# Kernel tuning notes

Measured on AMD Instinct MI355X. Metric: run time of the kernel, lower is better.

Reference implementation:

```python
import jax, jax.numpy as jnp
import numpy as np

XYZ_MIN = jnp.array([-1.0, -1.0, -1.0], dtype=jnp.float32)
XYZ_MAX = jnp.array([1.0, 1.0, 1.0], dtype=jnp.float32)
ACT_SHIFT = float(np.log(1.0 / (1.0 - 1e-6) - 1.0))  # density bias shift
WS = 100  # world_size per axis for num_voxels=1024000 in [-1,1]^3
R, P = 4096, 128  # rays, points per ray


def grid_sample_3d(grid, xyz):
    """Trilinear grid_sample, align_corners=True, zeros padding.
    grid: [C, D, H, W] (D=z, H=y, W=x); xyz: [N, 3] world coords. Returns [N, C]."""
    C, D, H, W = grid.shape
    norm = (xyz - XYZ_MIN) / (XYZ_MAX - XYZ_MIN) * 2.0 - 1.0  # [-1,1]
    sizes = jnp.array([W, H, D], dtype=norm.dtype)
    pix = (norm + 1.0) * 0.5 * (sizes - 1.0)  # align_corners=True mapping
    p0f = jnp.floor(pix)
    frac = pix - p0f
    p0 = p0f.astype(jnp.int32)
    out = jnp.zeros((xyz.shape[0], C), dtype=grid.dtype)
    for dx in (0, 1):
        for dy in (0, 1):
            for dz in (0, 1):
                ix, iy, iz = p0[:, 0] + dx, p0[:, 1] + dy, p0[:, 2] + dz
                wx = frac[:, 0] if dx else 1.0 - frac[:, 0]
                wy = frac[:, 1] if dy else 1.0 - frac[:, 1]
                wz = frac[:, 2] if dz else 1.0 - frac[:, 2]
                valid = ((ix >= 0) & (ix < W) & (iy >= 0) & (iy < H)
                         & (iz >= 0) & (iz < D))
                ixc = jnp.clip(ix, 0, W - 1)
                iyc = jnp.clip(iy, 0, H - 1)
                izc = jnp.clip(iz, 0, D - 1)
                vals = grid[:, izc, iyc, ixc].T  # [N, C]
                out = out + vals * (wx * wy * wz * valid)[:, None]
    return out


def setup_inputs() -> dict:
    key = jax.random.key(0)
    ks = jax.random.split(key, 12)
    origins = jax.random.uniform(ks[0], (R, 3), jnp.float32, -0.5, 0.5)
    directions = jax.random.normal(ks[1], (R, 3), jnp.float32)
    lengths = jax.random.uniform(ks[2], (R, P), jnp.float32, 0.05, 0.6)
    grid_density = jax.random.normal(ks[3], (1, WS, WS, WS), jnp.float32) * 0.1
    grid_color = jax.random.normal(ks[4], (12, WS, WS, WS), jnp.float32) * 0.1
    d_in = 12 + 27
    w1 = jax.random.normal(ks[5], (d_in, 128), jnp.float32) / np.sqrt(d_in)
    b1 = jnp.zeros((128,), jnp.float32)
    w2 = jax.random.normal(ks[6], (128, 128), jnp.float32) / np.sqrt(128)
    b2 = jnp.zeros((128,), jnp.float32)
    w3 = jax.random.normal(ks[7], (128, 3), jnp.float32) / np.sqrt(128)
    b3 = jnp.zeros((3,), jnp.float32)
    return dict(origins=origins, directions=directions, lengths=lengths,
                grid_density=grid_density, grid_color=grid_color,
                w1=w1, b1=b1, w2=w2, b2=b2, w3=w3, b3=b3)


def reference(origins, directions, lengths, grid_density, grid_color,
              w1, b1, w2, b2, w3, b3):
    # ray points: [R, P, 3]
    pts = origins[:, None, :] + directions[:, None, :] * lengths[:, :, None]
    flat = pts.reshape(-1, 3)
    # density branch
    density = grid_sample_3d(grid_density, flat).reshape(R, P, 1)
    interval = jnp.linalg.norm(directions, axis=-1)[:, None, None]
    alpha = 1.0 - (1.0 + jnp.exp(density + ACT_SHIFT)) ** (-interval)
    # color branch: 12-ch feature grid + view-dir PE + small MLP
    color = grid_sample_3d(grid_color, flat).reshape(R, P, 12)
    freqs = jnp.array([1.0, 2.0, 4.0, 8.0], dtype=jnp.float32)
    emb = (directions[:, :, None] * freqs).reshape(R, 12)
    emb = jnp.concatenate([directions, jnp.sin(emb), jnp.cos(emb)], -1)  # [R,27]
    emb = jnp.broadcast_to(emb[:, None, :], (R, P, 27))
    h = jnp.concatenate([color, emb], -1)  # [R,P,39]
    h = jax.nn.relu(h @ w1 + b1)
    h = jax.nn.relu(h @ w2 + b2)
    rgb = jax.nn.sigmoid(h @ w3 + b3)
    return alpha, rgb
```

## Files before the change

kernel.cpp:

```cpp
#include <hip/hip_runtime.h>
#include <hip/hip_bf16.h>
#include <math.h>


typedef __bf16 bf16x4 __attribute__((ext_vector_type(4)));
typedef __bf16 bf16x8 __attribute__((ext_vector_type(8)));
typedef float  f32x4  __attribute__((ext_vector_type(4)));

#define ACT_SHIFT_F (-13.815509557964774f)

#define EMB_B   53248
#define PACK_B  315392
#define FEAT_B  32315392
#define NEED_FULL 49092608ull
#define NEED_PACK 32315392ull

__global__ __launch_bounds__(256)
void dvgo_prep(const float* __restrict__ g_gd, const float* __restrict__ g_gc,
               const float* __restrict__ g_w1, const float* __restrict__ g_w2,
               const float* __restrict__ g_w3, const float* __restrict__ g_dir,
               bf16x8* __restrict__ pack, __bf16* __restrict__ wsb,
               __bf16* __restrict__ emb, int wbase)
{
    const int bid = blockIdx.x;
    if (bid < wbase) {
        const int gi = bid * 256 + threadIdx.x;
        if (gi >= 1000000) return;
        bf16x8 v0, v1;
        #pragma unroll
        for (int c = 0; c < 8; ++c) v0[c] = (__bf16)g_gc[c * 1000000 + gi];
        #pragma unroll
        for (int c = 0; c < 4; ++c) v1[c] = (__bf16)g_gc[(8 + c) * 1000000 + gi];
        v1[4] = (__bf16)g_gd[gi];
        v1[5] = (__bf16)0.0f; v1[6] = (__bf16)0.0f; v1[7] = (__bf16)0.0f;
        pack[gi * 2 + 0] = v0;
        pack[gi * 2 + 1] = v1;
        return;
    }
    const int idx = (bid - wbase) * 256 + threadIdx.x;
    if (idx < 8192) {
        const int j = idx & 7, lane = (idx >> 3) & 63, ks = (idx >> 9) & 1, ct = idx >> 10;
        const int n = ct * 16 + (lane & 15);
        const int k = ks * 32 + ((lane >> 4) & 3) * 8 + j;
        wsb[idx] = (__bf16)((k < 39) ? g_w1[k * 128 + n] : 0.0f);
    } else if (idx < 24576) {
        const int i2 = idx - 8192;
        const int j = i2 & 7, lane = (i2 >> 3) & 63, ks = (i2 >> 9) & 3, ct = i2 >> 11;
        const int n = ct * 16 + (lane & 15);
        const int k = ks * 32 + ((lane >> 4) & 3) * 8 + j;
        wsb[idx] = (__bf16)g_w2[k * 128 + n];
    } else if (idx < 26624) {
        const int i3 = idx - 24576;
        const int j = i3 & 7, lane = (i3 >> 3) & 63, ks = i3 >> 9;
        const int c = lane & 15;
        const int k = ks * 32 + ((lane >> 4) & 3) * 8 + j;
        wsb[idx] = (__bf16)((c < 3) ? g_w3[k * 3 + c] : 0.0f);
    } else if (idx < 30720) {
        const int ray = idx - 26624;
        const float d0 = g_dir[ray*3+0], d1 = g_dir[ray*3+1], d2 = g_dir[ray*3+2];
        __bf16 e[32];
        #pragma unroll
        for (int s = 0; s < 32; ++s) e[s] = (__bf16)0.0f;
        #pragma unroll
        for (int m = 0; m < 12; ++m) {
            const int i = m >> 2, j = m & 3;
            const float di = (i == 0) ? d0 : ((i == 1) ? d1 : d2);
            const float a = di * (float)(1 << j);
            if (m >= 1) e[m - 1] = (__bf16)sinf(a);
            e[11 + m] = (__bf16)cosf(a);
        }
        bf16x8* o = (bf16x8*)(emb + (size_t)ray * 32);
        #pragma unroll
        for (int q = 0; q < 4; ++q) {
            bf16x8 v;
            #pragma unroll
            for (int j = 0; j < 8; ++j) v[j] = e[q*8 + j];
            o[q] = v;
        }
    }
}

__global__ __launch_bounds__(256, 6)
void dvgo_gather(const float* __restrict__ g_org, const float* __restrict__ g_dir,
                 const float* __restrict__ g_len, const bf16x8* __restrict__ pack,
                 __bf16* __restrict__ feat, float* __restrict__ out_alpha)
{
    const int pt  = blockIdx.x * 256 + threadIdx.x;
    const int ray = pt >> 7;
    const float d0 = g_dir[ray*3+0], d1 = g_dir[ray*3+1], d2 = g_dir[ray*3+2];
    const float o0 = g_org[ray*3+0], o1 = g_org[ray*3+1], o2 = g_org[ray*3+2];
    const float len = g_len[pt];

    const float px = (o0 + d0*len + 1.0f) * 49.5f;
    const float py = (o1 + d1*len + 1.0f) * 49.5f;
    const float pz = (o2 + d2*len + 1.0f) * 49.5f;
    const float fx = floorf(px), fy = floorf(py), fz = floorf(pz);
    const int ix = (int)fx, iy = (int)fy, iz = (int)fz;
    const float qx = px - fx, qy = py - fy, qz = pz - fz;
    const float wxa[2] = {1.0f - qx, qx};
    const float wya[2] = {1.0f - qy, qy};
    const float wza[2] = {1.0f - qz, qz};
    const int  cxa[2] = {min(max(ix,0),99),   min(max(ix+1,0),99)};
    const int  cya[2] = {min(max(iy,0),99),   min(max(iy+1,0),99)};
    const int  cza[2] = {min(max(iz,0),99),   min(max(iz+1,0),99)};
    const bool vxa[2] = {(unsigned)ix < 100u, (unsigned)(ix+1) < 100u};
    const bool vya[2] = {(unsigned)iy < 100u, (unsigned)(iy+1) < 100u};
    const bool vza[2] = {(unsigned)iz < 100u, (unsigned)(iz+1) < 100u};

    float den = 0.0f;
    float cc[12];
    #pragma unroll
    for (int c = 0; c < 12; ++c) cc[c] = 0.0f;

    #pragma unroll
    for (int dz = 0; dz < 2; ++dz)
    #pragma unroll
    for (int dy = 0; dy < 2; ++dy)
    #pragma unroll
    for (int dx = 0; dx < 2; ++dx) {
        float w = wxa[dx] * wya[dy] * wza[dz];
        if (!(vxa[dx] && vya[dy] && vza[dz])) w = 0.0f;
        const int gi = (cza[dz]*100 + cya[dy])*100 + cxa[dx];
        const bf16x8 v0 = pack[gi*2 + 0];
        const bf16x8 v1 = pack[gi*2 + 1];
        #pragma unroll
        for (int c = 0; c < 8; ++c) cc[c]     += w * (float)v0[c];
        #pragma unroll
        for (int c = 0; c < 4; ++c) cc[8 + c] += w * (float)v1[c];
        den += w * (float)v1[4];
    }

    const float interval = sqrtf(d0*d0 + d1*d1 + d2*d2);
    const float e = expf(den + ACT_SHIFT_F);
    out_alpha[pt] = -expm1f(-interval * log1pf(e));

    bf16x8 f0, f1;
    #pragma unroll
    for (int c = 0; c < 8; ++c) f0[c] = (__bf16)cc[c];
    #pragma unroll
    for (int c = 0; c < 4; ++c) f1[c] = (__bf16)cc[8 + c];
    f1[4] = (__bf16)d0; f1[5] = (__bf16)d1; f1[6] = (__bf16)d2;
    f1[7] = (__bf16)sinf(d0);
    bf16x8* fo = (bf16x8*)(feat + (size_t)pt * 16);
    fo[0] = f0;
    fo[1] = f1;
}

__global__ __launch_bounds__(256, 3)
void dvgo_mlp(const bf16x8* __restrict__ wf, const __bf16* __restrict__ emb,
              const __bf16* __restrict__ feat,
              const float* __restrict__ g_b1, const float* __restrict__ g_b2,
              const float* __restrict__ g_b3, float* __restrict__ out_rgb)
{
    __shared__ __align__(16) char smem[32768];
    const int tid  = threadIdx.x;
    const int ray  = blockIdx.x;
    const int lane = tid & 63;
    const int wid  = tid >> 6;
    const int lr   = lane & 15;
    const int lk   = lane >> 4;
    const int sz   = (lr & 7) << 4;

    int wb1[2];
    #pragma unroll
    for (int c2 = 0; c2 < 2; ++c2)
        wb1[c2] = lr*256 + ((((wid*2 + c2)*32) + lk*8) ^ sz);
    int rb2[4];
    #pragma unroll
    for (int ks = 0; ks < 4; ++ks)
        rb2[ks] = (wid*32 + lr)*256 + ((ks*64 + lk*16) ^ sz);
    const int rowb = (wid*32 + lr)*256;

    const bf16x8 ev = *(const bf16x8*)(emb + (size_t)ray*32 + (((lk + 2) & 3) * 8));
    bf16x8 zed;
    #pragma unroll
    for (int j = 0; j < 8; ++j) zed[j] = (__bf16)0.0f;
    const bf16x8 bq1 = (lk < 2) ? ev : zed;

    bf16x8 aw1[2][2];
    #pragma unroll
    for (int c2 = 0; c2 < 2; ++c2)
        #pragma unroll
        for (int ks = 0; ks < 2; ++ks)
            aw1[c2][ks] = wf[((wid*2 + c2)*2 + ks)*64 + lane];

    #pragma unroll
    for (int h = 0; h < 2; ++h) {
        bf16x8 ft[4];
        #pragma unroll
        for (int r4 = 0; r4 < 4; ++r4) {
            const int pt = ray*128 + (h*4 + r4)*16 + lr;
            ft[r4] = *(const bf16x8*)(feat + (size_t)pt*16 + (lk & 1)*8);
        }
        f32x4 acc1[4][2];
        #pragma unroll
        for (int r4 = 0; r4 < 4; ++r4)
            #pragma unroll
            for (int c2 = 0; c2 < 2; ++c2) acc1[r4][c2] = (f32x4){0.f,0.f,0.f,0.f};
        #pragma unroll
        for (int r4 = 0; r4 < 4; ++r4) {
            const bf16x8 b0 = (lk < 2) ? ft[r4] : ev;
            #pragma unroll
            for (int c2 = 0; c2 < 2; ++c2) {
                acc1[r4][c2] = __builtin_amdgcn_mfma_f32_16x16x32_bf16(aw1[c2][0], b0,  acc1[r4][c2], 0, 0, 0);
                acc1[r4][c2] = __builtin_amdgcn_mfma_f32_16x16x32_bf16(aw1[c2][1], bq1, acc1[r4][c2], 0, 0, 0);
            }
        }
        #pragma unroll
        for (int c2 = 0; c2 < 2; ++c2) {
            const f32x4 b1v = *(const f32x4*)(g_b1 + (wid*2 + c2)*16 + lk*4);
            #pragma unroll
            for (int r4 = 0; r4 < 4; ++r4) {
                bf16x4 hv;
                #pragma unroll
                for (int r = 0; r < 4; ++r)
                    hv[r] = (__bf16)fmaxf(acc1[r4][c2][r] + b1v[r], 0.0f);
                *(bf16x4*)(smem + wb1[c2] + (h*4 + r4)*4096) = hv;
            }
        }
    }
    __syncthreads();

    bf16x8 hq[2][4];
    #pragma unroll
    for (int q = 0; q < 2; ++q)
        #pragma unroll
        for (int ks = 0; ks < 4; ++ks)
            hq[q][ks] = *(const bf16x8*)(smem + rb2[ks] + q*4096);

    #pragma unroll
    for (int ct = 0; ct < 8; ++ct) {
        bf16x8 aw2[4];
        #pragma unroll
        for (int ks = 0; ks < 4; ++ks)
            aw2[ks] = wf[1024 + (ct*4 + ks)*64 + lane];
        f32x4 a0 = (f32x4){0.f,0.f,0.f,0.f};
        f32x4 a1 = (f32x4){0.f,0.f,0.f,0.f};
        #pragma unroll
        for (int ks = 0; ks < 4; ++ks) {
            a0 = __builtin_amdgcn_mfma_f32_16x16x32_bf16(aw2[ks], hq[0][ks], a0, 0, 0, 0);
            a1 = __builtin_amdgcn_mfma_f32_16x16x32_bf16(aw2[ks], hq[1][ks], a1, 0, 0, 0);
        }
        const f32x4 b2v = *(const f32x4*)(g_b2 + ct*16 + lk*4);
        bf16x4 h0, h1;
        #pragma unroll
        for (int r = 0; r < 4; ++r) {
            h0[r] = (__bf16)fmaxf(a0[r] + b2v[r], 0.0f);
            h1[r] = (__bf16)fmaxf(a1[r] + b2v[r], 0.0f);
        }
        const int csw = (ct*32 + lk*8) ^ sz;
        *(bf16x4*)(smem + rowb + csw) = h0;
        *(bf16x4*)(smem + rowb + 4096 + csw) = h1;
    }

    bf16x8 aw3[4];
    #pragma unroll
    for (int ks = 0; ks < 4; ++ks) aw3[ks] = wf[3072 + ks*64 + lane];
    f32x4 acc3[2];
    acc3[0] = (f32x4){0.f,0.f,0.f,0.f};
    acc3[1] = (f32x4){0.f,0.f,0.f,0.f};
    #pragma unroll
    for (int q = 0; q < 2; ++q)
        #pragma unroll
        for (int ks = 0; ks < 4; ++ks) {
            const bf16x8 hq3 = *(const bf16x8*)(smem + rb2[ks] + q*4096);
            acc3[q] = __builtin_amdgcn_mfma_f32_16x16x32_bf16(aw3[ks], hq3, acc3[q], 0, 0, 0);
        }

    float* smf = (float*)(smem + wid*8192);
    if (lk == 0) {
        const float b30 = g_b3[0], b31 = g_b3[1], b32 = g_b3[2];
        #pragma unroll
        for (int q = 0; q < 2; ++q) {
            const int o = (q*16 + lr)*3;
            smf[o + 0] = 1.0f / (1.0f + __expf(-(acc3[q][0] + b30)));
            smf[o + 1] = 1.0f / (1.0f + __expf(-(acc3[q][1] + b31)));
            smf[o + 2] = 1.0f / (1.0f + __expf(-(acc3[q][2] + b32)));
        }
    }
    asm volatile("s_waitcnt lgkmcnt(0)");
    __builtin_amdgcn_sched_barrier(0);
    {
        const int base = (ray*128 + wid*32)*3;
        out_rgb[base + lane] = smf[lane];
        if (lane < 32) out_rgb[base + 64 + lane] = smf[64 + lane];
    }
}

#define FB_FEAT_OFF 0
#define FB_PCC_OFF  16384
#define FB_H1_OFF   0
#define FB_PRGB_OFF 0

template <bool PACKED>
__global__ __launch_bounds__(256, 4)
void dvgo_main(const float* __restrict__ g_org, const float* __restrict__ g_dir,
               const float* __restrict__ g_len, const float* __restrict__ g_gd,
               const float* __restrict__ g_gc, const float* __restrict__ g_b1,
               const float* __restrict__ g_b2, const float* __restrict__ g_w3,
               const float* __restrict__ g_b3, const bf16x8* __restrict__ wf,
               const bf16x8* __restrict__ g_pack,
               float* __restrict__ out_alpha, float* __restrict__ out_rgb)
{
    __shared__ __align__(16) char smem[32768];
    float* smf = (float*)smem;
    const int tid = threadIdx.x;
    const int ray = blockIdx.x;
    const float d0 = g_dir[ray*3+0], d1 = g_dir[ray*3+1], d2 = g_dir[ray*3+2];
    {
        const float o0 = g_org[ray*3+0], o1 = g_org[ray*3+1], o2 = g_org[ray*3+2];
        const int p = tid & 127;
        const int dzv = tid >> 7;
        const float len = g_len[ray*128 + p];
        const float px = (o0 + d0*len + 1.0f) * 49.5f;
        const float py = (o1 + d1*len + 1.0f) * 49.5f;
        const float pz = (o2 + d2*len + 1.0f) * 49.5f;
        const float fx = floorf(px), fy = floorf(py), fz = floorf(pz);
        const int ix = (int)fx, iy = (int)fy, iz0 = (int)fz;
        const float qx = px - fx, qy = py - fy, qz = pz - fz;
        const float wxa[2] = {1.0f - qx, qx};
        const float wya[2] = {1.0f - qy, qy};
        const int  cxa[2] = {min(max(ix,0),99),   min(max(ix+1,0),99)};
        const int  cya[2] = {min(max(iy,0),99),   min(max(iy+1,0),99)};
        const bool vxa[2] = {(unsigned)ix < 100u, (unsigned)(ix+1) < 100u};
        const bool vya[2] = {(unsigned)iy < 100u, (unsigned)(iy+1) < 100u};
        const int  iz = iz0 + dzv;
        const float wz = dzv ? qz : (1.0f - qz);
        const int  cz = min(max(iz,0),99);
        const bool vz = (unsigned)iz < 100u;
        float den = 0.0f;
        float cc[12];
        #pragma unroll
        for (int c = 0; c < 12; ++c) cc[c] = 0.0f;
        #pragma unroll
        for (int dy = 0; dy < 2; ++dy)
        #pragma unroll
        for (int dx = 0; dx < 2; ++dx) {
            float w = wxa[dx] * wya[dy] * wz;
            if (!(vxa[dx] && vya[dy] && vz)) w = 0.0f;
            const int gi = (cz*100 + cya[dy])*100 + cxa[dx];
            if (PACKED) {
                const bf16x8 v0 = g_pack[gi*2 + 0];
                const bf16x8 v1 = g_pack[gi*2 + 1];
                #pragma unroll
                for (int c = 0; c < 8; ++c) cc[c]     += w * (float)v0[c];
                #pragma unroll
                for (int c = 0; c < 4; ++c) cc[8 + c] += w * (float)v1[c];
                den += w * (float)v1[4];
            } else {
                den += w * g_gd[gi];
                #pragma unroll
                for (int c = 0; c < 12; ++c) cc[c] += w * g_gc[c*1000000 + gi];
            }
        }
        if (dzv) {
            #pragma unroll
            for (int c = 0; c < 12; ++c) smf[FB_PCC_OFF/4 + p*13 + c] = cc[c];
            smf[FB_PCC_OFF/4 + p*13 + 12] = den;
        }
        __syncthreads();
        if (!dzv) {
            #pragma unroll
            for (int c = 0; c < 12; ++c) cc[c] += smf[FB_PCC_OFF/4 + p*13 + c];
            den += smf[FB_PCC_OFF/4 + p*13 + 12];
            const float interval = sqrtf(d0*d0 + d1*d1 + d2*d2);
            const float e = expf(den + ACT_SHIFT_F);
            out_alpha[ray*128 + p] = -expm1f(-interval * log1pf(e));
            bf16x8 f0; bf16x4 f1;
            #pragma unroll
            for (int c = 0; c < 8; ++c) f0[c] = (__bf16)cc[c];
            #pragma unroll
            for (int c = 0; c < 4; ++c) f1[c] = (__bf16)cc[8+c];
            const int swz = (p & 7) << 4;
            *reinterpret_cast<bf16x8*>(smem + ((FB_FEAT_OFF + p*128 +  0) ^ swz)) = f0;
            *reinterpret_cast<bf16x4*>(smem + ((FB_FEAT_OFF + p*128 + 16) ^ swz)) = f1;
        } else {
            float vals[52];
            vals[0] = d0; vals[1] = d1; vals[2] = d2;
            #pragma unroll
            for (int i = 0; i < 3; ++i) {
                const float di = (i == 0) ? d0 : ((i == 1) ? d1 : d2);
                #pragma unroll
                for (int j = 0; j < 4; ++j) {
                    const float a = di * (float)(1 << j);
                    vals[3  + i*4 + j] = sinf(a);
                    vals[15 + i*4 + j] = cosf(a);
                }
            }
            #pragma unroll
            for (int c = 27; c < 52; ++c) vals[c] = 0.0f;
            const int swz = (p & 7) << 4;
            #pragma unroll
            for (int i = 0; i < 13; ++i) {
                bf16x4 v4;
                #pragma unroll
                for (int r = 0; r < 4; ++r) v4[r] = (__bf16)vals[i*4 + r];
                *reinterpret_cast<bf16x4*>(smem + ((FB_FEAT_OFF + p*128 + 24 + i*8) ^ swz)) = v4;
            }
        }
    }
    __syncthreads();
    const int lane = tid & 63;
    const int wid  = tid >> 6;
    const int lr   = lane & 15;
    const int lk   = lane >> 4;
    {
        bf16x8 bf[2][2];
        #pragma unroll
        for (int rt = 0; rt < 2; ++rt)
            #pragma unroll
            for (int ks = 0; ks < 2; ++ks) {
                const int pt = wid*32 + rt*16 + lr;
                int a = FB_FEAT_OFF + pt*128 + ks*64 + lk*16; a ^= (pt & 7) << 4;
                bf[rt][ks] = *reinterpret_cast<const bf16x8*>(smem + a);
            }
        __syncthreads();
        f32x4 acc1[2][8];
        #pragma unroll
        for (int rt = 0; rt < 2; ++rt)
            #pragma unroll
            for (int ct = 0; ct < 8; ++ct) acc1[rt][ct] = (f32x4){0.f,0.f,0.f,0.f};
        #pragma unroll
        for (int ct = 0; ct < 8; ++ct) {
            const bf16x8 aw0 = wf[(ct*2 + 0)*64 + lane];
            const bf16x8 aw1 = wf[(ct*2 + 1)*64 + lane];
            #pragma unroll
            for (int rt = 0; rt < 2; ++rt) {
                acc1[rt][ct] = __builtin_amdgcn_mfma_f32_16x16x32_bf16(aw0, bf[rt][0], acc1[rt][ct], 0, 0, 0);
                acc1[rt][ct] = __builtin_amdgcn_mfma_f32_16x16x32_bf16(aw1, bf[rt][1], acc1[rt][ct], 0, 0, 0);
            }
        }
        #pragma unroll
        for (int ct = 0; ct < 8; ++ct) {
            const f32x4 b1v = *reinterpret_cast<const f32x4*>(g_b1 + ct*16 + lk*4);
            #pragma unroll
            for (int rt = 0; rt < 2; ++rt) {
                const int pt = wid*32 + rt*16 + lr;
                bf16x4 hv;
                #pragma unroll
                for (int r = 0; r < 4; ++r)
                    hv[r] = (__bf16)fmaxf(acc1[rt][ct][r] + b1v[r], 0.0f);
                int a = FB_H1_OFF + pt*256 + ct*32 + lk*8; a ^= (pt & 7) << 4;
                *reinterpret_cast<bf16x4*>(smem + a) = hv;
            }
        }
    }
    __syncthreads();
    const int wr = wid >> 1, wc = wid & 1;
    f32x4 acc2[4][4];
    #pragma unroll
    for (int rt = 0; rt < 4; ++rt)
        #pragma unroll
        for (int ct = 0; ct < 4; ++ct) acc2[rt][ct] = (f32x4){0.f,0.f,0.f,0.f};
    #pragma unroll
    for (int ks = 0; ks < 4; ++ks) {
        bf16x8 a2[4];
        #pragma unroll
        for (int rt = 0; rt < 4; ++rt) {
            const int pt = wr*64 + rt*16 + lr;
            int a = FB_H1_OFF + pt*256 + ks*64 + lk*16; a ^= (pt & 7) << 4;
            a2[rt] = *reinterpret_cast<const bf16x8*>(smem + a);
        }
        #pragma unroll
        for (int ct = 0; ct < 4; ++ct) {
            const int ctg = wc*4 + ct;
            const bf16x8 b2f = wf[1024 + (ctg*4 + ks)*64 + lane];
            #pragma unroll
            for (int rt = 0; rt < 4; ++rt)
                acc2[rt][ct] = __builtin_amdgcn_mfma_f32_16x16x32_bf16(a2[rt], b2f, acc2[rt][ct], 0, 0, 0);
        }
    }
    __syncthreads();
    {
        float b2v[4], w30[4], w31[4], w32[4];
        #pragma unroll
        for (int ct = 0; ct < 4; ++ct) {
            const int n2 = wc*64 + ct*16 + lr;
            b2v[ct] = g_b2[n2];
            w30[ct] = g_w3[n2*3 + 0];
            w31[ct] = g_w3[n2*3 + 1];
            w32[ct] = g_w3[n2*3 + 2];
        }
        #pragma unroll
        for (int rt = 0; rt < 4; ++rt)
            #pragma unroll
            for (int r = 0; r < 4; ++r) {
                float s0 = 0.f, s1 = 0.f, s2 = 0.f;
                #pragma unroll
                for (int ct = 0; ct < 4; ++ct) {
                    const float v = fmaxf(acc2[rt][ct][r] + b2v[ct], 0.0f);
                    s0 = fmaf(v, w30[ct], s0);
                    s1 = fmaf(v, w31[ct], s1);
                    s2 = fmaf(v, w32[ct], s2);
                }
                #pragma unroll
                for (int off = 1; off < 16; off <<= 1) {
                    s0 += __shfl_xor(s0, off);
                    s1 += __shfl_xor(s1, off);
                    s2 += __shfl_xor(s2, off);
                }
                if (lr == 0) {
                    const int pt = wr*64 + rt*16 + lk*4 + r;
                    const int base = FB_PRGB_OFF/4 + (wc*128 + pt)*3;
                    smf[base + 0] = s0;
                    smf[base + 1] = s1;
                    smf[base + 2] = s2;
                }
            }
    }
    __syncthreads();
    if (tid < 128) {
        const int p = tid;
        const float s0 = smf[p*3 + 0] + smf[(128 + p)*3 + 0] + g_b3[0];
        const float s1 = smf[p*3 + 1] + smf[(128 + p)*3 + 1] + g_b3[1];
        const float s2 = smf[p*3 + 2] + smf[(128 + p)*3 + 2] + g_b3[2];
        const int pt = ray*128 + p;
        out_rgb[pt*3 + 0] = 1.0f / (1.0f + expf(-s0));
        out_rgb[pt*3 + 1] = 1.0f / (1.0f + expf(-s1));
        out_rgb[pt*3 + 2] = 1.0f / (1.0f + expf(-s2));
    }
}

extern "C" void kernel_launch(void* const* d_in, const int* in_sizes, int n_in,
                              void* d_out, int out_size, void* d_ws, size_t ws_size,
                              hipStream_t stream)
{
    const float* g_org = (const float*)d_in[0];
    const float* g_dir = (const float*)d_in[1];
    const float* g_len = (const float*)d_in[2];
    const float* g_gd  = (const float*)d_in[3];
    const float* g_gc  = (const float*)d_in[4];
    const float* g_w1  = (const float*)d_in[5];
    const float* g_b1  = (const float*)d_in[6];
    const float* g_w2  = (const float*)d_in[7];
    const float* g_b2  = (const float*)d_in[8];
    const float* g_w3  = (const float*)d_in[9];
    const float* g_b3  = (const float*)d_in[10];
    float* out = (float*)d_out;

    __bf16* wsb  = (__bf16*)d_ws;
    __bf16* emb  = (__bf16*)((char*)d_ws + EMB_B);
    bf16x8* pack = (bf16x8*)((char*)d_ws + PACK_B);

    if (ws_size >= NEED_FULL) {
        __bf16* feat = (__bf16*)((char*)d_ws + FEAT_B);
        dvgo_prep<<<4027, 256, 0, stream>>>(g_gd, g_gc, g_w1, g_w2, g_w3, g_dir,
                                            pack, wsb, emb, 3907);
        dvgo_gather<<<2048, 256, 0, stream>>>(g_org, g_dir, g_len, pack, feat, out);
        dvgo_mlp<<<4096, 256, 0, stream>>>((const bf16x8*)wsb, emb, feat,
                                           g_b1, g_b2, g_b3, out + 4096*128);
    } else if (ws_size >= NEED_PACK) {
        dvgo_prep<<<4011, 256, 0, stream>>>(g_gd, g_gc, g_w1, g_w2, g_w3, g_dir,
                                            pack, wsb, emb, 3907);
        dvgo_main<true><<<4096, 256, 0, stream>>>(g_org, g_dir, g_len, g_gd, g_gc,
                                                  g_b1, g_b2, g_w3, g_b3,
                                                  (const bf16x8*)wsb, pack,
                                                  out, out + 4096*128);
    } else {
        dvgo_prep<<<104, 256, 0, stream>>>(g_gd, g_gc, g_w1, g_w2, g_w3, g_dir,
                                           pack, wsb, emb, 0);
        dvgo_main<false><<<4096, 256, 0, stream>>>(g_org, g_dir, g_len, g_gd, g_gc,
                                                   g_b1, g_b2, g_w3, g_b3,
                                                   (const bf16x8*)wsb, nullptr,
                                                   out, out + 4096*128);
    }
}
```

Before: 77.28 us.

## Fold per-ray view-direction embedding into layer-1 bias and shrink feature records

Precomputes, per ray, the contribution of the positional-encoded view direction through w1 plus b1 as a float bias vector in the prep kernel. The MLP's first layer then multiplies only the 12 grid features, halving its MFMA count, and the gathered feature record shrinks from 16 to 12 bf16 values to cut memory traffic. It adds 4096×128 dot-product work in prep with sin/cos evaluations, and the 24-byte records make the vector loads unaligned. MLP occupancy hint is raised to 4 blocks.

```diff
diff --git a/kernel.cpp b/kernel.cpp
--- a/kernel.cpp
+++ b/kernel.cpp
@@ -9,22 +9,27 @@
 
 #define ACT_SHIFT_F (-13.815509557964774f)
 
+#define B1R_B   45056
+#define PACK2_B 2142208
+#define FEAT2_B 34142208
+#define NEED_FULL 46725120ull
+
 #define EMB_B   53248
 #define PACK_B  315392
-#define FEAT_B  32315392
-#define NEED_FULL 49092608ull
 #define NEED_PACK 32315392ull
 
 __global__ __launch_bounds__(256)
-void dvgo_prep(const float* __restrict__ g_gd, const float* __restrict__ g_gc,
-               const float* __restrict__ g_w1, const float* __restrict__ g_w2,
-               const float* __restrict__ g_w3, const float* __restrict__ g_dir,
-               bf16x8* __restrict__ pack, __bf16* __restrict__ wsb,
-               __bf16* __restrict__ emb, int wbase)
+void dvgo_prep2(const float* __restrict__ g_gd, const float* __restrict__ g_gc,
+                const float* __restrict__ g_w1, const float* __restrict__ g_w2,
+                const float* __restrict__ g_w3, const float* __restrict__ g_dir,
+                const float* __restrict__ g_b1,
+                bf16x8* __restrict__ pack, __bf16* __restrict__ wsb,
+                float* __restrict__ b1r)
 {
     const int bid = blockIdx.x;
-    if (bid < wbase) {
-        const int gi = bid * 256 + threadIdx.x;
+    const int tid = threadIdx.x;
+    if (bid < 3907) {
+        const int gi = bid * 256 + tid;
         if (gi >= 1000000) return;
         bf16x8 v0, v1;
         #pragma unroll
@@ -37,47 +42,44 @@
         pack[gi * 2 + 1] = v1;
         return;
     }
-    const int idx = (bid - wbase) * 256 + threadIdx.x;
-    if (idx < 8192) {
-        const int j = idx & 7, lane = (idx >> 3) & 63, ks = (idx >> 9) & 1, ct = idx >> 10;
-        const int n = ct * 16 + (lane & 15);
-        const int k = ks * 32 + ((lane >> 4) & 3) * 8 + j;
-        wsb[idx] = (__bf16)((k < 39) ? g_w1[k * 128 + n] : 0.0f);
-    } else if (idx < 24576) {
-        const int i2 = idx - 8192;
-        const int j = i2 & 7, lane = (i2 >> 3) & 63, ks = (i2 >> 9) & 3, ct = i2 >> 11;
-        const int n = ct * 16 + (lane & 15);
-        const int k = ks * 32 + ((lane >> 4) & 3) * 8 + j;
-        wsb[idx] = (__bf16)g_w2[k * 128 + n];
-    } else if (idx < 26624) {
-        const int i3 = idx - 24576;
-        const int j = i3 & 7, lane = (i3 >> 3) & 63, ks = i3 >> 9;
-        const int c = lane & 15;
-        const int k = ks * 32 + ((lane >> 4) & 3) * 8 + j;
-        wsb[idx] = (__bf16)((c < 3) ? g_w3[k * 3 + c] : 0.0f);
-    } else if (idx < 30720) {
-        const int ray = idx - 26624;
-        const float d0 = g_dir[ray*3+0], d1 = g_dir[ray*3+1], d2 = g_dir[ray*3+2];
-        __bf16 e[32];
-        #pragma unroll
-        for (int s = 0; s < 32; ++s) e[s] = (__bf16)0.0f;
-        #pragma unroll
-        for (int m = 0; m < 12; ++m) {
-            const int i = m >> 2, j = m & 3;
-            const float di = (i == 0) ? d0 : ((i == 1) ? d1 : d2);
-            const float a = di * (float)(1 << j);
-            if (m >= 1) e[m - 1] = (__bf16)sinf(a);
-            e[11 + m] = (__bf16)cosf(a);
-        }
-        bf16x8* o = (bf16x8*)(emb + (size_t)ray * 32);
-        #pragma unroll
-        for (int q = 0; q < 4; ++q) {
-            bf16x8 v;
-            #pragma unroll
-            for (int j = 0; j < 8; ++j) v[j] = e[q*8 + j];
-            o[q] = v;
-        }
-    }
+    const int idx2 = bid - 3907;
+    if (idx2 < 88) {
+        const int idx = idx2 * 256 + tid;
+        if (idx < 4096) {
+            const int j = idx & 7, lane = (idx >> 3) & 63, ct = idx >> 9;
+            const int n = ct * 16 + (lane & 15);
+            const int k = ((lane >> 4) & 3) * 8 + j;
+            wsb[idx] = (__bf16)((k < 12) ? g_w1[k * 128 + n] : 0.0f);
+        } else if (idx < 20480) {
+            const int i2 = idx - 4096;
+            const int j = i2 & 7, lane = (i2 >> 3) & 63, ks = (i2 >> 9) & 3, ct = i2 >> 11;
+            const int n = ct * 16 + (lane & 15);
+            const int k = ks * 32 + ((lane >> 4) & 3) * 8 + j;
+            wsb[idx] = (__bf16)g_w2[k * 128 + n];
+        } else if (idx < 22528) {
+            const int i3 = idx - 20480;
+            const int j = i3 & 7, lane = (i3 >> 3) & 63, ks = i3 >> 9;
+            const int c = lane & 15;
+            const int k = ks * 32 + ((lane >> 4) & 3) * 8 + j;
+            wsb[idx] = (__bf16)((c < 3) ? g_w3[k * 3 + c] : 0.0f);
+        }
+        return;
+    }
+    const int rr  = idx2 - 88;
+    const int ray = rr * 2 + (tid >> 7);
+    const int n   = tid & 127;
+    const float d0 = g_dir[ray*3+0], d1 = g_dir[ray*3+1], d2 = g_dir[ray*3+2];
+    float s = g_b1[n];
+    s += d0 * g_w1[12*128 + n] + d1 * g_w1[13*128 + n] + d2 * g_w1[14*128 + n];
+    #pragma unroll
+    for (int m = 0; m < 12; ++m) {
+        const int i = m >> 2, j = m & 3;
+        const float di = (i == 0) ? d0 : ((i == 1) ? d1 : d2);
+        const float a = di * (float)(1 << j);
+        s += sinf(a) * g_w1[(15 + m)*128 + n];
+        s += cosf(a) * g_w1[(27 + m)*128 + n];
+    }
+    b1r[ray*128 + n] = s;
 }
 
 __global__ __launch_bounds__(256, 6)
@@ -134,23 +136,21 @@
     const float e = expf(den + ACT_SHIFT_F);
     out_alpha[pt] = -expm1f(-interval * log1pf(e));
 
-    bf16x8 f0, f1;
+    bf16x8 f0; bf16x4 f1;
     #pragma unroll
     for (int c = 0; c < 8; ++c) f0[c] = (__bf16)cc[c];
     #pragma unroll
     for (int c = 0; c < 4; ++c) f1[c] = (__bf16)cc[8 + c];
-    f1[4] = (__bf16)d0; f1[5] = (__bf16)d1; f1[6] = (__bf16)d2;
-    f1[7] = (__bf16)sinf(d0);
-    bf16x8* fo = (bf16x8*)(feat + (size_t)pt * 16);
-    fo[0] = f0;
-    fo[1] = f1;
+    __bf16* fo = feat + (size_t)pt * 12;
+    *(bf16x8*)(fo) = f0;
+    *(bf16x4*)(fo + 8) = f1;
 }
 
-__global__ __launch_bounds__(256, 3)
-void dvgo_mlp(const bf16x8* __restrict__ wf, const __bf16* __restrict__ emb,
+__global__ __launch_bounds__(256, 4)
+void dvgo_mlp(const bf16x8* __restrict__ wf, const float* __restrict__ b1r,
               const __bf16* __restrict__ feat,
-              const float* __restrict__ g_b1, const float* __restrict__ g_b2,
-              const float* __restrict__ g_b3, float* __restrict__ out_rgb)
+              const float* __restrict__ g_b2, const float* __restrict__ g_b3,
+              float* __restrict__ out_rgb)
 {
     __shared__ __align__(16) char smem[32768];
     const int tid  = threadIdx.x;
@@ -171,26 +171,29 @@
         rb2[ks] = (wid*32 + lr)*256 + ((ks*64 + lk*16) ^ sz);
     const int rowb = (wid*32 + lr)*256;
 
-    const bf16x8 ev = *(const bf16x8*)(emb + (size_t)ray*32 + (((lk + 2) & 3) * 8));
     bf16x8 zed;
     #pragma unroll
     for (int j = 0; j < 8; ++j) zed[j] = (__bf16)0.0f;
-    const bf16x8 bq1 = (lk < 2) ? ev : zed;
-
-    bf16x8 aw1[2][2];
+
+    bf16x8 aw1[2];
     #pragma unroll
     for (int c2 = 0; c2 < 2; ++c2)
-        #pragma unroll
-        for (int ks = 0; ks < 2; ++ks)
-            aw1[c2][ks] = wf[((wid*2 + c2)*2 + ks)*64 + lane];
+        aw1[c2] = wf[(wid*2 + c2)*64 + lane];
 
     #pragma unroll
     for (int h = 0; h < 2; ++h) {
-        bf16x8 ft[4];
+        bf16x8 bb[4];
         #pragma unroll
         for (int r4 = 0; r4 < 4; ++r4) {
             const int pt = ray*128 + (h*4 + r4)*16 + lr;
-            ft[r4] = *(const bf16x8*)(feat + (size_t)pt*16 + (lk & 1)*8);
+            const bf16x8 t0 = *(const bf16x8*)(feat + (size_t)pt*12);
+            const bf16x4 t1 = *(const bf16x4*)(feat + (size_t)pt*12 + 8);
+            bf16x8 tl;
+            #pragma unroll
+            for (int j = 0; j < 4; ++j) tl[j] = t1[j];
+            #pragma unroll
+            for (int j = 4; j < 8; ++j) tl[j] = (__bf16)0.0f;
+            bb[r4] = (lk == 0) ? t0 : ((lk == 1) ? tl : zed);
         }
         f32x4 acc1[4][2];
         #pragma unroll
@@ -198,17 +201,13 @@
             #pragma unroll
             for (int c2 = 0; c2 < 2; ++c2) acc1[r4][c2] = (f32x4){0.f,0.f,0.f,0.f};
         #pragma unroll
-        for (int r4 = 0; r4 < 4; ++r4) {
-            const bf16x8 b0 = (lk < 2) ? ft[r4] : ev;
-            #pragma unroll
-            for (int c2 = 0; c2 < 2; ++c2) {
-                acc1[r4][c2] = __builtin_amdgcn_mfma_f32_16x16x32_bf16(aw1[c2][0], b0,  acc1[r4][c2], 0, 0, 0);
-                acc1[r4][c2] = __builtin_amdgcn_mfma_f32_16x16x32_bf16(aw1[c2][1], bq1, acc1[r4][c2], 0, 0, 0);
-            }
-        }
+        for (int r4 = 0; r4 < 4; ++r4)
+            #pragma unroll
+            for (int c2 = 0; c2 < 2; ++c2)
+                acc1[r4][c2] = __builtin_amdgcn_mfma_f32_16x16x32_bf16(aw1[c2], bb[r4], acc1[r4][c2], 0, 0, 0);
         #pragma unroll
         for (int c2 = 0; c2 < 2; ++c2) {
-            const f32x4 b1v = *(const f32x4*)(g_b1 + (wid*2 + c2)*16 + lk*4);
+            const f32x4 b1v = *(const f32x4*)(b1r + ray*128 + (wid*2 + c2)*16 + lk*4);
             #pragma unroll
             for (int r4 = 0; r4 < 4; ++r4) {
                 bf16x4 hv;
@@ -233,7 +232,7 @@
         bf16x8 aw2[4];
         #pragma unroll
         for (int ks = 0; ks < 4; ++ks)
-            aw2[ks] = wf[1024 + (ct*4 + ks)*64 + lane];
+            aw2[ks] = wf[512 + (ct*4 + ks)*64 + lane];
         f32x4 a0 = (f32x4){0.f,0.f,0.f,0.f};
         f32x4 a1 = (f32x4){0.f,0.f,0.f,0.f};
         #pragma unroll
@@ -255,7 +254,7 @@
 
     bf16x8 aw3[4];
     #pragma unroll
-    for (int ks = 0; ks < 4; ++ks) aw3[ks] = wf[3072 + ks*64 + lane];
+    for (int ks = 0; ks < 4; ++ks) aw3[ks] = wf[2560 + ks*64 + lane];
     f32x4 acc3[2];
     acc3[0] = (f32x4){0.f,0.f,0.f,0.f};
     acc3[1] = (f32x4){0.f,0.f,0.f,0.f};
@@ -284,6 +283,42 @@
         const int base = (ray*128 + wid*32)*3;
         out_rgb[base + lane] = smf[lane];
         if (lane < 32) out_rgb[base + 64 + lane] = smf[64 + lane];
+    }
+}
+
+__global__ __launch_bounds__(256)
+void dvgo_prep_fb(const float* __restrict__ g_gd, const float* __restrict__ g_gc,
+                  const float* __restrict__ g_w1, const float* __restrict__ g_w2,
+                  const float* __restrict__ g_w3, const float* __restrict__ g_dir,
+                  bf16x8* __restrict__ pack, __bf16* __restrict__ wsb, int wbase)
+{
+    const int bid = blockIdx.x;
+    if (bid < wbase) {
+        const int gi = bid * 256 + threadIdx.x;
+        if (gi >= 1000000) return;
+        bf16x8 v0, v1;
+        #pragma unroll
+        for (int c = 0; c < 8; ++c) v0[c] = (__bf16)g_gc[c * 1000000 + gi];
+        #pragma unroll
+        for (int c = 0; c < 4; ++c) v1[c] = (__bf16)g_gc[(8 + c) * 1000000 + gi];
+        v1[4] = (__bf16)g_gd[gi];
+        v1[5] = (__bf16)0.0f; v1[6] = (__bf16)0.0f; v1[7] = (__bf16)0.0f;
+        pack[gi * 2 + 0] = v0;
+        pack[gi * 2 + 1] = v1;
+        return;
+    }
+    const int idx = (bid - wbase) * 256 + threadIdx.x;
+    if (idx < 8192) {
+        const int j = idx & 7, lane = (idx >> 3) & 63, ks = (idx >> 9) & 1, ct = idx >> 10;
+        const int n = ct * 16 + (lane & 15);
+        const int k = ks * 32 + ((lane >> 4) & 3) * 8 + j;
+        wsb[idx] = (__bf16)((k < 39) ? g_w1[k * 128 + n] : 0.0f);
+    } else if (idx < 24576) {
+        const int i2 = idx - 8192;
+        const int j = i2 & 7, lane = (i2 >> 3) & 63, ks = (i2 >> 9) & 3, ct = i2 >> 11;
+        const int n = ct * 16 + (lane & 15);
+        const int k = ks * 32 + ((lane >> 4) & 3) * 8 + j;
+        wsb[idx] = (__bf16)g_w2[k * 128 + n];
     }
 }
 
@@ -538,27 +573,29 @@
     const float* g_b3  = (const float*)d_in[10];
     float* out = (float*)d_out;
 
-    __bf16* wsb  = (__bf16*)d_ws;
-    __bf16* emb  = (__bf16*)((char*)d_ws + EMB_B);
-    bf16x8* pack = (bf16x8*)((char*)d_ws + PACK_B);
-
     if (ws_size >= NEED_FULL) {
-        __bf16* feat = (__bf16*)((char*)d_ws + FEAT_B);
-        dvgo_prep<<<4027, 256, 0, stream>>>(g_gd, g_gc, g_w1, g_w2, g_w3, g_dir,
-                                            pack, wsb, emb, 3907);
+        __bf16* wsb  = (__bf16*)d_ws;
+        float*  b1r  = (float*)((char*)d_ws + B1R_B);
+        bf16x8* pack = (bf16x8*)((char*)d_ws + PACK2_B);
+        __bf16* feat = (__bf16*)((char*)d_ws + FEAT2_B);
+        dvgo_prep2<<<6043, 256, 0, stream>>>(g_gd, g_gc, g_w1, g_w2, g_w3, g_dir,
+                                             g_b1, pack, wsb, b1r);
         dvgo_gather<<<2048, 256, 0, stream>>>(g_org, g_dir, g_len, pack, feat, out);
-        dvgo_mlp<<<4096, 256, 0, stream>>>((const bf16x8*)wsb, emb, feat,
-                                           g_b1, g_b2, g_b3, out + 4096*128);
+        dvgo_mlp<<<4096, 256, 0, stream>>>((const bf16x8*)wsb, b1r, feat,
+                                           g_b2, g_b3, out + 4096*128);
     } else if (ws_size >= NEED_PACK) {
-        dvgo_prep<<<4011, 256, 0, stream>>>(g_gd, g_gc, g_w1, g_w2, g_w3, g_dir,
-                                            pack, wsb, emb, 3907);
+        __bf16* wsb  = (__bf16*)d_ws;
+        bf16x8* pack = (bf16x8*)((char*)d_ws + EMB_B);
+        dvgo_prep_fb<<<4011, 256, 0, stream>>>(g_gd, g_gc, g_w1, g_w2, g_w3, g_dir,
+                                               pack, wsb, 3907);
         dvgo_main<true><<<4096, 256, 0, stream>>>(g_org, g_dir, g_len, g_gd, g_gc,
                                                   g_b1, g_b2, g_w3, g_b3,
                                                   (const bf16x8*)wsb, pack,
                                                   out, out + 4096*128);
     } else {
-        dvgo_prep<<<104, 256, 0, stream>>>(g_gd, g_gc, g_w1, g_w2, g_w3, g_dir,
-                                           pack, wsb, emb, 0);
+        __bf16* wsb = (__bf16*)d_ws;
+        dvgo_prep_fb<<<104, 256, 0, stream>>>(g_gd, g_gc, g_w1, g_w2, g_w3, g_dir,
+                                              (bf16x8*)d_ws, wsb, 0);
         dvgo_main<false><<<4096, 256, 0, stream>>>(g_org, g_dir, g_len, g_gd, g_gc,
                                                    g_b1, g_b2, g_w3, g_b3,
                                                    (const bf16x8*)wsb, nullptr,
```

Result: slower. 83.74 us (+8.4%).
